# Optimization experiments

Measured on AMD Instinct MI355X. Metric: run time of the kernel, lower is better.

## Reference

```python
import jax, jax.numpy as jnp
import numpy as np

EPS = 1e-08

def rms_norm(x, eps=EPS):
    # Matches torch: mean-centered, population variance (unbiased=False)
    mean = jnp.mean(x, axis=-1, keepdims=True)
    var = jnp.var(x, axis=-1, keepdims=True)
    return (x - mean) / jnp.sqrt(var + eps)

def activation_quant(x):
    s = 127.0 / jnp.max(jnp.abs(x), axis=-1, keepdims=True)
    return jnp.clip(jnp.round(s * x), -128, 127) / s

def ternary_matmul(x, w):
    # pos_mask - neg_mask of sign(w) equals sign(w); x @ sign(w).T
    return jnp.matmul(x, jnp.sign(w).T)

def setup_inputs() -> dict:
    key = jax.random.key(0)
    k0, k1, k2, k3 = jax.random.split(key, 4)
    B, S, D, H = 4, 2048, 2048, 8192
    x = jax.random.normal(k0, (B, S, D), dtype=jnp.float32)
    W_g = jax.random.normal(k1, (H, D), dtype=jnp.float32) * 0.01
    W_u = jax.random.normal(k2, (H, D), dtype=jnp.float32) * 0.01
    W_d = jax.random.normal(k3, (D, H), dtype=jnp.float32) * 0.01
    return {"x": x, "W_g": W_g, "W_u": W_u, "W_d": W_d}

def reference(x, W_g, W_u, W_d):
    xq = activation_quant(rms_norm(x))
    g = jax.nn.silu(ternary_matmul(xq, W_g))   # [B,S,H]
    u = ternary_matmul(xq, W_u)                # [B,S,H]
    p = g * u
    return ternary_matmul(p, W_d)              # [B,S,D]
```

## Files before the change

kernel.cpp:

```cpp
#include <hip/hip_runtime.h>
#include <stdint.h>

#define MROWS 8192
#define DDIM  2048
#define HDIM  8192

typedef __attribute__((ext_vector_type(8))) short bf16x8;
typedef __attribute__((ext_vector_type(4))) float f32x4;
typedef __attribute__((ext_vector_type(4))) int   i32x4;
typedef unsigned short u16;

__device__ __forceinline__ void async_load16(const void* g, void* l) {
  auto gp = reinterpret_cast<const __attribute__((address_space(1))) unsigned int*>(
      reinterpret_cast<uintptr_t>(g));
  auto lp = reinterpret_cast<__attribute__((address_space(3))) unsigned int*>(
      reinterpret_cast<uintptr_t>(l));
  __builtin_amdgcn_global_load_lds(gp, lp, 16, 0, 0);
}

__device__ __forceinline__ u16 f2bf(float f) {
  union { float f; unsigned int u; } v; v.f = f;
  unsigned int r = v.u + 0x7FFF + ((v.u >> 16) & 1);
  return (u16)(r >> 16);
}

__global__ void sign_i8x2_kernel(const float* __restrict__ wg, const float* __restrict__ wu,
                                 char* __restrict__ og, char* __restrict__ ou) {
  const int t = blockIdx.x * 256 + threadIdx.x;
  const float* w = blockIdx.y ? wu : wg;
  char* o = blockIdx.y ? ou : og;
  const float4* w4 = (const float4*)w;
  float4 a = w4[t * 2], b = w4[t * 2 + 1];
  float v[8] = {a.x, a.y, a.z, a.w, b.x, b.y, b.z, b.w};
  union { char s[8]; uint2 u; } pk;
#pragma unroll
  for (int i = 0; i < 8; i++)
    pk.s[i] = v[i] > 0.f ? (char)1 : (v[i] < 0.f ? (char)-1 : (char)0);
  ((uint2*)o)[t] = pk.u;
}

__global__ void sign_bf16_kernel(const float* __restrict__ w, u16* __restrict__ o) {
  const int t = blockIdx.x * 256 + threadIdx.x;
  const float4* w4 = (const float4*)w;
  float4 a = w4[t * 2], b = w4[t * 2 + 1];
  float v[8] = {a.x, a.y, a.z, a.w, b.x, b.y, b.z, b.w};
  union { u16 s[8]; uint4 u; } pk;
#pragma unroll
  for (int i = 0; i < 8; i++)
    pk.s[i] = v[i] > 0.f ? 0x3F80 : (v[i] < 0.f ? 0xBF80 : 0);
  ((uint4*)o)[t] = pk.u;
}

__global__ void norm_quant_i8_kernel(const float* __restrict__ x,
                                     char* __restrict__ q, float* __restrict__ inv) {
  const int row  = blockIdx.x;
  const int tid  = threadIdx.x;
  const int lane = tid & 63, wave = tid >> 6;
  const float4* xr = (const float4*)(x + (size_t)row * DDIM);
  float4 a = xr[tid * 2], b = xr[tid * 2 + 1];
  float v[8] = {a.x, a.y, a.z, a.w, b.x, b.y, b.z, b.w};
  float s1 = 0.f, s2 = 0.f;
#pragma unroll
  for (int i = 0; i < 8; i++) { s1 += v[i]; s2 += v[i] * v[i]; }
#pragma unroll
  for (int o = 1; o < 64; o <<= 1) { s1 += __shfl_xor(s1, o); s2 += __shfl_xor(s2, o); }
  __shared__ float ssum[4], ssq[4], smax[4];
  if (lane == 0) { ssum[wave] = s1; ssq[wave] = s2; }
  __syncthreads();
  s1 = ssum[0] + ssum[1] + ssum[2] + ssum[3];
  s2 = ssq[0] + ssq[1] + ssq[2] + ssq[3];
  const float mean = s1 * (1.f / DDIM);
  const float var  = s2 * (1.f / DDIM) - mean * mean;
  const float rstd = rsqrtf(var + 1e-8f);
  float mx = 0.f;
#pragma unroll
  for (int i = 0; i < 8; i++) { v[i] = (v[i] - mean) * rstd; mx = fmaxf(mx, fabsf(v[i])); }
#pragma unroll
  for (int o = 1; o < 64; o <<= 1) mx = fmaxf(mx, __shfl_xor(mx, o));
  if (lane == 0) smax[wave] = mx;
  __syncthreads();
  mx = fmaxf(fmaxf(smax[0], smax[1]), fmaxf(smax[2], smax[3]));
  const float s = 127.f / mx;
  if (tid == 0) inv[row] = mx * (1.f / 127.f);
  union { char s8[8]; uint2 u; } pk;
#pragma unroll
  for (int i = 0; i < 8; i++) {
    float qq = rintf(v[i] * s);
    qq = fminf(fmaxf(qq, -128.f), 127.f);
    pk.s8[i] = (char)(int)qq;
  }
  ((uint2*)(q + (size_t)row * DDIM))[tid] = pk.u;
}

__global__ __launch_bounds__(256, 2) void gemm_glu_i8_kernel(
    const char* __restrict__ A,
    const char* __restrict__ Bg,
    const char* __restrict__ Bu,
    const float* __restrict__ inv,
    u16* __restrict__ P)
{
  constexpr int K = DDIM;
  const int l   = blockIdx.x + gridDim.x * blockIdx.y;
  const int xcd = l & 7;
  const int s_  = l >> 3;
  const int n0 = (xcd * 8 + (s_ & 7)) * 128;
  const int m0 = (s_ >> 3) * 128;
  const int tid  = threadIdx.x;
  const int lane = tid & 63, wave = tid >> 6;
  const int wm = wave >> 1, wn = wave & 1;
  const int quad = lane >> 4, l16 = lane & 15;

  __shared__ __align__(16) char lds[49152];
  char* lA  = lds;
  char* lBg = lds + 16384;
  char* lBu = lds + 32768;

  i32x4 accg[4][4], accu[4][4];
  const i32x4 zero = {0, 0, 0, 0};
#pragma unroll
  for (int i = 0; i < 4; i++)
#pragma unroll
    for (int j = 0; j < 4; j++) { accg[i][j] = zero; accu[i][j] = zero; }

  const int arow = wm * 64 + l16;
  const int brow = wn * 64 + l16;
  const int aswz = (arow & 7) << 4;
  const int bswz = (brow & 7) << 4;

  for (int k0 = 0; k0 < K; k0 += 128) {
    __syncthreads();
#pragma unroll
    for (int is = 0; is < 4; ++is) {
      const int o   = is * 4096 + tid * 16;
      const int r   = o >> 7;
      const int cbs = (o & 127) ^ ((r & 7) << 4);
      async_load16(A  + (size_t)(m0 + r) * K + k0 + cbs, lA  + is * 4096 + wave * 1024);
      async_load16(Bg + (size_t)(n0 + r) * K + k0 + cbs, lBg + is * 4096 + wave * 1024);
      async_load16(Bu + (size_t)(n0 + r) * K + k0 + cbs, lBu + is * 4096 + wave * 1024);
    }
    __syncthreads();
#pragma unroll
    for (int ks = 0; ks < 2; ++ks) {
      const int koff = ks * 64 + quad * 16;
      i32x4 a[4], bg[4], bu[4];
#pragma unroll
      for (int i = 0; i < 4; i++)
        a[i] = *(const i32x4*)(lA + (arow + i * 16) * 128 + (koff ^ aswz));
#pragma unroll
      for (int j = 0; j < 4; j++) {
        bg[j] = *(const i32x4*)(lBg + (brow + j * 16) * 128 + (koff ^ bswz));
        bu[j] = *(const i32x4*)(lBu + (brow + j * 16) * 128 + (koff ^ bswz));
      }
#pragma unroll
      for (int i = 0; i < 4; i++)
#pragma unroll
        for (int j = 0; j < 4; j++) {
          accg[i][j] = __builtin_amdgcn_mfma_i32_16x16x64_i8(a[i], bg[j], accg[i][j], 0, 0, 0);
          accu[i][j] = __builtin_amdgcn_mfma_i32_16x16x64_i8(a[i], bu[j], accu[i][j], 0, 0, 0);
        }
    }
  }

  const int rbase = m0 + wm * 64 + quad * 4;
  const int cbase = n0 + wn * 64 + l16;
#pragma unroll
  for (int i = 0; i < 4; i++) {
    float iv[4];
#pragma unroll
    for (int r = 0; r < 4; r++) iv[r] = inv[rbase + i * 16 + r];
#pragma unroll
    for (int j = 0; j < 4; j++)
#pragma unroll
      for (int r = 0; r < 4; r++) {
        float g = (float)accg[i][j][r] * iv[r];
        float u = (float)accu[i][j][r] * iv[r];
        float pv = (g / (1.f + __expf(-g))) * u;
        P[(size_t)(rbase + i * 16 + r) * HDIM + (cbase + j * 16)] = f2bf(pv);
      }
  }
}

__global__ __launch_bounds__(256, 4) void gemm_out_kernel(
    const u16* __restrict__ A,
    const u16* __restrict__ B,
    float* __restrict__ C)
{
  constexpr int K = HDIM;
  const int l   = blockIdx.x + gridDim.x * blockIdx.y;
  const int xcd = l & 7;
  const int s_  = l >> 3;
  const int n0 = ((xcd & 1) * 8 + (s_ & 7)) * 128;
  const int m0 = ((xcd >> 1) * 16 + (s_ >> 3)) * 128;
  const int tid  = threadIdx.x;
  const int lane = tid & 63, wave = tid >> 6;
  const int wm = wave >> 1, wn = wave & 1;
  const int quad = lane >> 4, l16 = lane & 15;

  __shared__ __align__(16) char lds[32768];
  char* lA = lds;
  char* lB = lds + 16384;

  f32x4 acc[4][4];
  const f32x4 zero = {0.f, 0.f, 0.f, 0.f};
#pragma unroll
  for (int i = 0; i < 4; i++)
#pragma unroll
    for (int j = 0; j < 4; j++) acc[i][j] = zero;

  const int arow = wm * 64 + l16;
  const int brow = wn * 64 + l16;
  const int aswz = (arow & 7) << 4;
  const int bswz = (brow & 7) << 4;

  for (int k0 = 0; k0 < K; k0 += 64) {
    __syncthreads();
#pragma unroll
    for (int is = 0; is < 4; ++is) {
      const int o   = is * 4096 + tid * 16;
      const int r   = o >> 7;
      const int cbs = (o & 127) ^ ((r & 7) << 4);
      async_load16((const char*)A + ((size_t)(m0 + r) * K + k0) * 2 + cbs, lA + is * 4096 + wave * 1024);
      async_load16((const char*)B + ((size_t)(n0 + r) * K + k0) * 2 + cbs, lB + is * 4096 + wave * 1024);
    }
    __syncthreads();
#pragma unroll
    for (int ks = 0; ks < 2; ++ks) {
      const int koff = ks * 64 + quad * 16;
      bf16x8 a[4], b[4];
#pragma unroll
      for (int i = 0; i < 4; i++)
        a[i] = *(const bf16x8*)(lA + (arow + i * 16) * 128 + (koff ^ aswz));
#pragma unroll
      for (int j = 0; j < 4; j++)
        b[j] = *(const bf16x8*)(lB + (brow + j * 16) * 128 + (koff ^ bswz));
#pragma unroll
      for (int i = 0; i < 4; i++)
#pragma unroll
        for (int j = 0; j < 4; j++)
          acc[i][j] = __builtin_amdgcn_mfma_f32_16x16x32_bf16(a[i], b[j], acc[i][j], 0, 0, 0);
    }
  }

  const int rbase = m0 + wm * 64 + quad * 4;
  const int cbase = n0 + wn * 64 + l16;
#pragma unroll
  for (int i = 0; i < 4; i++)
#pragma unroll
    for (int j = 0; j < 4; j++)
#pragma unroll
      for (int r = 0; r < 4; r++)
        C[(size_t)(rbase + i * 16 + r) * DDIM + (cbase + j * 16)] = acc[i][j][r];
}

extern "C" void kernel_launch(void* const* d_in, const int* in_sizes, int n_in,
                              void* d_out, int out_size, void* d_ws, size_t ws_size,
                              hipStream_t stream) {
  const float* x  = (const float*)d_in[0];
  const float* Wg = (const float*)d_in[1];
  const float* Wu = (const float*)d_in[2];
  const float* Wd = (const float*)d_in[3];

  char* ws = (char*)d_ws;
  char*  q    = ws;
  float* inv  = (float*)(ws + 16777216ull);
  char*  sWg  = ws + 20971520ull;
  char*  sWu  = ws + 37748736ull;
  u16*   sWd  = (u16*)(ws + 54525952ull);
  u16*   p    = (u16*)(ws + 88080384ull);
  float* out  = (float*)d_out;

  dim3 gs(8192, 2);
  sign_i8x2_kernel<<<gs, 256, 0, stream>>>(Wg, Wu, sWg, sWu);
  sign_bf16_kernel<<<8192, 256, 0, stream>>>(Wd, sWd);

  norm_quant_i8_kernel<<<MROWS, 256, 0, stream>>>(x, q, inv);

  dim3 g1(HDIM / 128, MROWS / 128);
  gemm_glu_i8_kernel<<<g1, 256, 0, stream>>>(q, sWg, sWu, inv, p);

  dim3 g2(DDIM / 128, MROWS / 128);
  gemm_out_kernel<<<g2, 256, 0, stream>>>(p, sWd, out);
}
```

Before: 735.6 us.

## Double-buffer LDS with 512-thread blocks and larger tiles in both GEMMs

```diff
diff --git a/kernel.cpp b/kernel.cpp
--- a/kernel.cpp
+++ b/kernel.cpp
@@ -92,28 +92,26 @@
   ((uint2*)(q + (size_t)row * DDIM))[tid] = pk.u;
 }
 
-__global__ __launch_bounds__(256, 2) void gemm_glu_i8_kernel(
+__global__ __launch_bounds__(512, 2) void gemm_glu_i8_kernel(
     const char* __restrict__ A,
     const char* __restrict__ Bg,
     const char* __restrict__ Bu,
     const float* __restrict__ inv,
     u16* __restrict__ P)
 {
-  constexpr int K = DDIM;
+  constexpr int K  = DDIM;
+  constexpr int NT = K / 128;
   const int l   = blockIdx.x + gridDim.x * blockIdx.y;
   const int xcd = l & 7;
   const int s_  = l >> 3;
   const int n0 = (xcd * 8 + (s_ & 7)) * 128;
-  const int m0 = (s_ >> 3) * 128;
+  const int m0 = (s_ >> 3) * 256;
   const int tid  = threadIdx.x;
   const int lane = tid & 63, wave = tid >> 6;
   const int wm = wave >> 1, wn = wave & 1;
   const int quad = lane >> 4, l16 = lane & 15;
 
-  __shared__ __align__(16) char lds[49152];
-  char* lA  = lds;
-  char* lBg = lds + 16384;
-  char* lBu = lds + 32768;
+  __shared__ __align__(16) char lds[131072];
 
   i32x4 accg[4][4], accu[4][4];
   const i32x4 zero = {0, 0, 0, 0};
@@ -124,42 +122,76 @@
 
   const int arow = wm * 64 + l16;
   const int brow = wn * 64 + l16;
-  const int aswz = (arow & 7) << 4;
-  const int bswz = (brow & 7) << 4;
-
-  for (int k0 = 0; k0 < K; k0 += 128) {
-    __syncthreads();
-#pragma unroll
-    for (int is = 0; is < 4; ++is) {
-      const int o   = is * 4096 + tid * 16;
-      const int r   = o >> 7;
-      const int cbs = (o & 127) ^ ((r & 7) << 4);
-      async_load16(A  + (size_t)(m0 + r) * K + k0 + cbs, lA  + is * 4096 + wave * 1024);
-      async_load16(Bg + (size_t)(n0 + r) * K + k0 + cbs, lBg + is * 4096 + wave * 1024);
-      async_load16(Bu + (size_t)(n0 + r) * K + k0 + cbs, lBu + is * 4096 + wave * 1024);
+  const int swz  = (l16 & 7) << 4;
+
+  const int rr  = tid >> 3;
+  const int cbs = ((tid & 7) << 4) ^ ((rr & 7) << 4);
+  const char* aSrc = A  + (size_t)(m0 + rr) * K + cbs;
+  const char* gSrc = Bg + (size_t)(n0 + rr) * K + cbs;
+  const char* uSrc = Bu + (size_t)(n0 + rr) * K + cbs;
+
+#define STG_A(is) async_load16(aSrc + (size_t)(is) * 64 * K + k0n, bufN + (is) * 8192 + wave * 1024)
+#define STG_G(is) async_load16(gSrc + (size_t)(is) * 64 * K + k0n, bufN + 32768 + (is) * 8192 + wave * 1024)
+#define STG_U(is) async_load16(uSrc + (size_t)(is) * 64 * K + k0n, bufN + 49152 + (is) * 8192 + wave * 1024)
+
+  {
+    char* bufN = lds;
+    const int k0n = 0;
+    STG_A(0); STG_A(1); STG_A(2); STG_A(3);
+    STG_G(0); STG_G(1); STG_U(0); STG_U(1);
+    asm volatile("s_waitcnt vmcnt(0)" ::: "memory");
+    __builtin_amdgcn_s_barrier();
+  }
+
+  for (int t = 0; t < NT; ++t) {
+    const char* bufC = lds + (size_t)(t & 1) * 65536;
+    char* bufN = lds + (size_t)((t + 1) & 1) * 65536;
+    const int k0n = (t + 1) * 128;
+    const bool pre = (t + 1) < NT;
+    i32x4 a[4];
+#pragma unroll
+    for (int ks = 0; ks < 2; ++ks) {
+#pragma unroll
+      for (int jh = 0; jh < 2; ++jh) {
+        const int koff = (ks * 64 + quad * 16) ^ swz;
+        if (jh == 0) {
+#pragma unroll
+          for (int i = 0; i < 4; ++i)
+            a[i] = *(const i32x4*)(bufC + (size_t)(arow + i * 16) * 128 + koff);
+        }
+        i32x4 bg[2], bu[2];
+#pragma unroll
+        for (int jj = 0; jj < 2; ++jj) {
+          const int j = jh * 2 + jj;
+          bg[jj] = *(const i32x4*)(bufC + 32768 + (size_t)(brow + j * 16) * 128 + koff);
+          bu[jj] = *(const i32x4*)(bufC + 49152 + (size_t)(brow + j * 16) * 128 + koff);
+        }
+        const int ph = ks * 2 + jh;
+        if (pre) {
+          if (ph == 0)      { STG_A(0); STG_A(1); STG_A(2); }
+          else if (ph == 1) { STG_A(3); STG_G(0); STG_G(1); }
+          else if (ph == 2) { STG_U(0); STG_U(1); }
+        }
+        __builtin_amdgcn_s_barrier();
+        asm volatile("s_waitcnt lgkmcnt(0)" ::: "memory");
+        __builtin_amdgcn_s_setprio(1);
+#pragma unroll
+        for (int i = 0; i < 4; ++i)
+#pragma unroll
+          for (int jj = 0; jj < 2; ++jj) {
+            const int j = jh * 2 + jj;
+            accg[i][j] = __builtin_amdgcn_mfma_i32_16x16x64_i8(a[i], bg[jj], accg[i][j], 0, 0, 0);
+            accu[i][j] = __builtin_amdgcn_mfma_i32_16x16x64_i8(a[i], bu[jj], accu[i][j], 0, 0, 0);
+          }
+        __builtin_amdgcn_s_setprio(0);
+        if (ph == 3) asm volatile("s_waitcnt vmcnt(0)" ::: "memory");
+        __builtin_amdgcn_s_barrier();
+      }
     }
-    __syncthreads();
-#pragma unroll
-    for (int ks = 0; ks < 2; ++ks) {
-      const int koff = ks * 64 + quad * 16;
-      i32x4 a[4], bg[4], bu[4];
-#pragma unroll
-      for (int i = 0; i < 4; i++)
-        a[i] = *(const i32x4*)(lA + (arow + i * 16) * 128 + (koff ^ aswz));
-#pragma unroll
-      for (int j = 0; j < 4; j++) {
-        bg[j] = *(const i32x4*)(lBg + (brow + j * 16) * 128 + (koff ^ bswz));
-        bu[j] = *(const i32x4*)(lBu + (brow + j * 16) * 128 + (koff ^ bswz));
-      }
-#pragma unroll
-      for (int i = 0; i < 4; i++)
-#pragma unroll
-        for (int j = 0; j < 4; j++) {
-          accg[i][j] = __builtin_amdgcn_mfma_i32_16x16x64_i8(a[i], bg[j], accg[i][j], 0, 0, 0);
-          accu[i][j] = __builtin_amdgcn_mfma_i32_16x16x64_i8(a[i], bu[j], accu[i][j], 0, 0, 0);
-        }
-    }
-  }
+  }
+#undef STG_A
+#undef STG_G
+#undef STG_U
 
   const int rbase = m0 + wm * 64 + quad * 4;
   const int cbase = n0 + wn * 64 + l16;
@@ -180,71 +212,102 @@
   }
 }
 
-__global__ __launch_bounds__(256, 4) void gemm_out_kernel(
+__global__ __launch_bounds__(512, 2) void gemm_out_kernel(
     const u16* __restrict__ A,
     const u16* __restrict__ B,
     float* __restrict__ C)
 {
-  constexpr int K = HDIM;
+  constexpr size_t KB = (size_t)HDIM * 2;
+  constexpr int NT = (int)(KB / 128);
   const int l   = blockIdx.x + gridDim.x * blockIdx.y;
   const int xcd = l & 7;
   const int s_  = l >> 3;
-  const int n0 = ((xcd & 1) * 8 + (s_ & 7)) * 128;
-  const int m0 = ((xcd >> 1) * 16 + (s_ >> 3)) * 128;
+  const int n0 = xcd * 256;
+  const int m0 = s_ * 256;
   const int tid  = threadIdx.x;
   const int lane = tid & 63, wave = tid >> 6;
-  const int wm = wave >> 1, wn = wave & 1;
+  const int wm = wave >> 2, wn = wave & 3;
   const int quad = lane >> 4, l16 = lane & 15;
 
-  __shared__ __align__(16) char lds[32768];
-  char* lA = lds;
-  char* lB = lds + 16384;
-
-  f32x4 acc[4][4];
+  __shared__ __align__(16) char lds[131072];
+
+  f32x4 acc[8][4];
   const f32x4 zero = {0.f, 0.f, 0.f, 0.f};
 #pragma unroll
-  for (int i = 0; i < 4; i++)
+  for (int i = 0; i < 8; i++)
 #pragma unroll
     for (int j = 0; j < 4; j++) acc[i][j] = zero;
 
-  const int arow = wm * 64 + l16;
+  const int arow = wm * 128 + l16;
   const int brow = wn * 64 + l16;
-  const int aswz = (arow & 7) << 4;
-  const int bswz = (brow & 7) << 4;
-
-  for (int k0 = 0; k0 < K; k0 += 64) {
-    __syncthreads();
-#pragma unroll
-    for (int is = 0; is < 4; ++is) {
-      const int o   = is * 4096 + tid * 16;
-      const int r   = o >> 7;
-      const int cbs = (o & 127) ^ ((r & 7) << 4);
-      async_load16((const char*)A + ((size_t)(m0 + r) * K + k0) * 2 + cbs, lA + is * 4096 + wave * 1024);
-      async_load16((const char*)B + ((size_t)(n0 + r) * K + k0) * 2 + cbs, lB + is * 4096 + wave * 1024);
+  const int swz  = (l16 & 7) << 4;
+
+  const int rr  = tid >> 3;
+  const int cbs = ((tid & 7) << 4) ^ ((rr & 7) << 4);
+  const char* aSrc = (const char*)A + (size_t)(m0 + rr) * KB + cbs;
+  const char* bSrc = (const char*)B + (size_t)(n0 + rr) * KB + cbs;
+
+#define STG2_A(is) async_load16(aSrc + (size_t)(is) * 64 * KB + k0n, bufN + (is) * 8192 + wave * 1024)
+#define STG2_B(is) async_load16(bSrc + (size_t)(is) * 64 * KB + k0n, bufN + 32768 + (is) * 8192 + wave * 1024)
+
+  {
+    char* bufN = lds;
+    const int k0n = 0;
+    STG2_A(0); STG2_A(1); STG2_A(2); STG2_A(3);
+    STG2_B(0); STG2_B(1); STG2_B(2); STG2_B(3);
+    asm volatile("s_waitcnt vmcnt(0)" ::: "memory");
+    __builtin_amdgcn_s_barrier();
+  }
+
+  for (int t = 0; t < NT; ++t) {
+    const char* bufC = lds + (size_t)(t & 1) * 65536;
+    char* bufN = lds + (size_t)((t + 1) & 1) * 65536;
+    const int k0n = (t + 1) * 128;
+    const bool pre = (t + 1) < NT;
+    bf16x8 b[4];
+#pragma unroll
+    for (int ks = 0; ks < 2; ++ks) {
+#pragma unroll
+      for (int ih = 0; ih < 2; ++ih) {
+        const int koff = (ks * 64 + quad * 16) ^ swz;
+        if (ih == 0) {
+#pragma unroll
+          for (int j = 0; j < 4; ++j)
+            b[j] = *(const bf16x8*)(bufC + 32768 + (size_t)(brow + j * 16) * 128 + koff);
+        }
+        bf16x8 a[4];
+#pragma unroll
+        for (int ii = 0; ii < 4; ++ii)
+          a[ii] = *(const bf16x8*)(bufC + (size_t)(arow + (ih * 4 + ii) * 16) * 128 + koff);
+        const int ph = ks * 2 + ih;
+        if (pre) {
+          if (ph == 0)      { STG2_A(0); STG2_A(1); STG2_A(2); }
+          else if (ph == 1) { STG2_A(3); STG2_B(0); STG2_B(1); }
+          else if (ph == 2) { STG2_B(2); STG2_B(3); }
+        }
+        __builtin_amdgcn_s_barrier();
+        asm volatile("s_waitcnt lgkmcnt(0)" ::: "memory");
+        __builtin_amdgcn_s_setprio(1);
+#pragma unroll
+        for (int ii = 0; ii < 4; ++ii) {
+          const int i = ih * 4 + ii;
+#pragma unroll
+          for (int j = 0; j < 4; ++j)
+            acc[i][j] = __builtin_amdgcn_mfma_f32_16x16x32_bf16(a[ii], b[j], acc[i][j], 0, 0, 0);
+        }
+        __builtin_amdgcn_s_setprio(0);
+        if (ph == 3) asm volatile("s_waitcnt vmcnt(0)" ::: "memory");
+        __builtin_amdgcn_s_barrier();
+      }
     }
-    __syncthreads();
-#pragma unroll
-    for (int ks = 0; ks < 2; ++ks) {
-      const int koff = ks * 64 + quad * 16;
-      bf16x8 a[4], b[4];
-#pragma unroll
-      for (int i = 0; i < 4; i++)
-        a[i] = *(const bf16x8*)(lA + (arow + i * 16) * 128 + (koff ^ aswz));
-#pragma unroll
-      for (int j = 0; j < 4; j++)
-        b[j] = *(const bf16x8*)(lB + (brow + j * 16) * 128 + (koff ^ bswz));
-#pragma unroll
-      for (int i = 0; i < 4; i++)
-#pragma unroll
-        for (int j = 0; j < 4; j++)
-          acc[i][j] = __builtin_amdgcn_mfma_f32_16x16x32_bf16(a[i], b[j], acc[i][j], 0, 0, 0);
-    }
-  }
-
-  const int rbase = m0 + wm * 64 + quad * 4;
+  }
+#undef STG2_A
+#undef STG2_B
+
+  const int rbase = m0 + wm * 128 + quad * 4;
   const int cbase = n0 + wn * 64 + l16;
 #pragma unroll
-  for (int i = 0; i < 4; i++)
+  for (int i = 0; i < 8; i++)
 #pragma unroll
     for (int j = 0; j < 4; j++)
 #pragma unroll
@@ -275,9 +338,9 @@
 
   norm_quant_i8_kernel<<<MROWS, 256, 0, stream>>>(x, q, inv);
 
-  dim3 g1(HDIM / 128, MROWS / 128);
-  gemm_glu_i8_kernel<<<g1, 256, 0, stream>>>(q, sWg, sWu, inv, p);
-
-  dim3 g2(DDIM / 128, MROWS / 128);
-  gemm_out_kernel<<<g2, 256, 0, stream>>>(p, sWd, out);
-}
+  dim3 g1(HDIM / 128, MROWS / 256);
+  gemm_glu_i8_kernel<<<g1, 512, 0, stream>>>(q, sWg, sWu, inv, p);
+
+  dim3 g2(DDIM / 256, MROWS / 256);
+  gemm_out_kernel<<<g2, 512, 0, stream>>>(p, sWd, out);
+}
```

After: 785.4 us. 6.8% more time.
